# Performance work log

Hardware: AMD Instinct MI355X
Metric: run time of the kernel (lower is better)

Reference implementation:

```python
import jax, jax.numpy as jnp
import numpy as np

B, S, E = 2, 2048, 2048
H = 16
KV_RANK = 512
ROPE = 64
NOPE = 64  # source sets qk_nope_dim = qk_rope_dim
VD = 128   # v_head_dim = head_dim
QD = ROPE + NOPE  # q_head_dim = 128


def setup_inputs() -> dict:
    key = jax.random.key(0)
    ks = jax.random.split(key, 5)
    sd = lambda fan_in: 1.0 / np.sqrt(fan_in)
    return {
        "x": jax.random.normal(ks[0], (B, S, E), jnp.float32),
        "attention_mask": jnp.zeros((1, 1, S, S), jnp.float32),
        "W_kv_down": jax.random.normal(ks[1], (KV_RANK + ROPE, E), jnp.float32) * sd(E),
        "W_kv_up": jax.random.normal(ks[2], (H * (VD + NOPE), KV_RANK), jnp.float32) * sd(KV_RANK),
        "W_q": jax.random.normal(ks[3], (H * QD, E), jnp.float32) * sd(E),
        "W_out": jax.random.normal(ks[4], (E, H * VD), jnp.float32) * sd(H * VD),
    }


def reference(x, attention_mask, W_kv_down, W_kv_up, W_q, W_out):
    scale = QD ** (-0.5)
    # down-project to latent + rope part
    compressed = jnp.einsum('bse,fe->bsf', x, W_kv_down)          # [B,S,KV_RANK+ROPE]
    kv_c, k_rope = compressed[..., :KV_RANK], compressed[..., KV_RANK:]
    # up-project latent to per-head v and k_nope
    kv_exp = jnp.einsum('bsr,fr->bsf', kv_c, W_kv_up)             # [B,S,H*(VD+NOPE)]
    kv_exp = kv_exp.reshape(B, S, H, VD + NOPE).transpose(0, 2, 1, 3)  # [B,H,S,VD+NOPE]
    v, k_nope = kv_exp[..., :VD], kv_exp[..., VD:]
    # shared rope key broadcast over heads, concat [rope, nope]
    k_rope_b = jnp.broadcast_to(k_rope[:, None], (B, H, S, ROPE))
    k = jnp.concatenate([k_rope_b, k_nope], axis=-1)              # [B,H,S,QD]
    # queries
    q = jnp.einsum('bse,fe->bsf', x, W_q).reshape(B, S, H, QD).transpose(0, 2, 1, 3)
    scores = jnp.einsum('bhsd,bhtd->bhst', q, k) * scale + attention_mask
    w = jax.nn.softmax(scores, axis=-1)
    out = jnp.einsum('bhst,bhtv->bhsv', w, v)                     # [B,H,S,VD]
    out = out.transpose(0, 2, 1, 3).reshape(B, S, H * VD)
    return jnp.einsum('bsf,ef->bse', out, W_out)
```

## Files before the change

kernel.cpp:

```cpp
#include <hip/hip_runtime.h>
#include <hip/hip_bf16.h>
#include <stdint.h>

typedef __bf16 bf16x8 __attribute__((ext_vector_type(8)));
typedef float f32x4 __attribute__((ext_vector_type(4)));
typedef unsigned short ushort_t;
typedef unsigned short ushort8v __attribute__((ext_vector_type(8)));

#define MFMA16 __builtin_amdgcn_mfma_f32_16x16x32_bf16

static constexpr int Bc = 2, Sc = 2048, Ec = 2048, Hc = 16;

__device__ __forceinline__ void gload16(const void* g, void* l) {
  __builtin_amdgcn_global_load_lds(
      (const __attribute__((address_space(1))) void*)g,
      (__attribute__((address_space(3))) void*)l, 16, 0, 0);
}

__device__ __forceinline__ ushort_t f2bf(float f) {
  uint32_t u = __float_as_uint(f);
  uint32_t r = (u + 0x7fffu + ((u >> 16) & 1u)) >> 16;
  return (ushort_t)r;
}
__device__ __forceinline__ float bf2f(ushort_t u) {
  return __uint_as_float((uint32_t)u << 16);
}
__device__ __forceinline__ uint32_t cvtpk(float a, float b) {
  uint32_t d;
  asm("v_cvt_pk_bf16_f32 %0, %1, %2" : "=v"(d) : "v"(a), "v"(b));
  return d;
}

__global__ void cast_all(const float* __restrict__ x, const float* __restrict__ Wq,
                         const float* __restrict__ Wkvu, const float* __restrict__ Wout,
                         const float* __restrict__ Wkvd,
                         ushort_t* __restrict__ xb, ushort_t* __restrict__ wq,
                         ushort_t* __restrict__ wkvu, ushort_t* __restrict__ wout,
                         ushort_t* __restrict__ wkvd) {
  int i = blockIdx.x * 256 + threadIdx.x;
  const float* src;
  ushort_t* dst;
  int j;
  if (i < 2097152) { src = x; dst = xb; j = i; }
  else if (i < 3145728) { src = Wq; dst = wq; j = i - 2097152; }
  else if (i < 3538944) { src = Wkvu; dst = wkvu; j = i - 3145728; }
  else if (i < 4587520) { src = Wout; dst = wout; j = i - 3538944; }
  else {
    j = i - 4587520;
    int row = j >> 9, col4 = j & 511;
    ushort4 o;
    if (row < 576) {
      float4 v = ((const float4*)Wkvd)[row * 512 + col4];
      o.x = f2bf(v.x); o.y = f2bf(v.y); o.z = f2bf(v.z); o.w = f2bf(v.w);
    } else { o.x = 0; o.y = 0; o.z = 0; o.w = 0; }
    ((ushort4*)wkvd)[j] = o;
    return;
  }
  float4 v = ((const float4*)src)[j];
  ushort4 o;
  o.x = f2bf(v.x); o.y = f2bf(v.y); o.z = f2bf(v.z); o.w = f2bf(v.w);
  ((ushort4*)dst)[j] = o;
}

__global__ void mask_rearrange(const float* __restrict__ mask, ushort_t* __restrict__ m3) {
  const float INVLN2 = 1.4426950408889634f;
  int i = blockIdx.x * 256 + threadIdx.x;
  if (i >= 524288) return;
  int half = i & 1, g = (i >> 1) & 3, kt = (i >> 3) & 31, q = i >> 8;
  const float* s0 = mask + (size_t)q * 2048 + kt * 64 + half * 32 + g * 4;
  float4 a = *(const float4*)s0;
  float4 c = *(const float4*)(s0 + 16);
  ushort8v o;
  o[0] = f2bf(a.x * INVLN2); o[1] = f2bf(a.y * INVLN2);
  o[2] = f2bf(a.z * INVLN2); o[3] = f2bf(a.w * INVLN2);
  o[4] = f2bf(c.x * INVLN2); o[5] = f2bf(c.y * INVLN2);
  o[6] = f2bf(c.z * INVLN2); o[7] = f2bf(c.w * INVLN2);
  ((ushort8v*)m3)[i] = o;
}

template<int MODE>
__global__ __launch_bounds__(256, 2)
void gemm_bt(const ushort_t* __restrict__ A, int lda,
             const ushort_t* __restrict__ Bm, int ldb,
             void* __restrict__ Cout, int ldc,
             int M, int N, int K,
             char* __restrict__ vtb, char* __restrict__ kbuf)
{
  __shared__ __align__(16) ushort_t sA[128 * 32];
  __shared__ __align__(16) ushort_t sB[128 * 32];
  int tid = threadIdx.x;
  int nTn = N >> 7;
  int bid = blockIdx.x;
  int chunk = gridDim.x >> 3;
  bid = (bid & 7) * chunk + (bid >> 3);
  int tm = bid / nTn, tn = bid - tm * nTn;
  int wave = tid >> 6, lane = tid & 63;
  int wm = (wave >> 1) << 6, wn = (wave & 1) << 6;
  int l16 = lane & 15, g16 = lane >> 4;
  f32x4 acc[4][4] = {};
  int srow = tid >> 2, scol = (tid & 3) << 3;
  const ushort_t* Ag = A + (size_t)(tm * 128 + srow) * lda + scol;
  const ushort_t* Bg = Bm + (size_t)(tn * 128 + srow) * ldb + scol;
  ushort_t* sAp = &sA[srow * 32 + scol];
  ushort_t* sBp = &sB[srow * 32 + scol];
  for (int kt = 0; kt < K; kt += 32) {
    gload16(Ag, sAp);
    gload16(Ag + (size_t)64 * lda, sAp + 64 * 32);
    gload16(Bg, sBp);
    gload16(Bg + (size_t)64 * ldb, sBp + 64 * 32);
    Ag += 32; Bg += 32;
    __syncthreads();
    bf16x8 af[4], bfr[4];
#pragma unroll
    for (int i = 0; i < 4; i++) af[i] = *(const bf16x8*)&sA[(wm + i * 16 + l16) * 32 + g16 * 8];
#pragma unroll
    for (int i = 0; i < 4; i++) bfr[i] = *(const bf16x8*)&sB[(wn + i * 16 + l16) * 32 + g16 * 8];
#pragma unroll
    for (int i = 0; i < 4; i++)
#pragma unroll
      for (int j = 0; j < 4; j++)
        acc[i][j] = MFMA16(af[i], bfr[j], acc[i][j], 0, 0, 0);
    __syncthreads();
  }
#pragma unroll
  for (int i = 0; i < 4; i++) {
#pragma unroll
    for (int j = 0; j < 4; j++) {
#pragma unroll
      for (int r = 0; r < 4; r++) {
        int grow = tm * 128 + wm + i * 16 + g16 * 4 + r;
        int gcol = tn * 128 + wn + j * 16 + l16;
        float v = acc[i][j][r];
        if constexpr (MODE == 0) {
          ((ushort_t*)Cout)[(size_t)grow * ldc + gcol] = f2bf(v);
        } else if constexpr (MODE == 2) {
          ((float*)Cout)[(size_t)grow * ldc + gcol] = v;
        } else {
          int h = gcol / 192, jj = gcol - h * 192;
          int b = grow >> 11, s = grow & 2047;
          size_t bh = (size_t)(b * Hc + h);
          if (jj < 128) {
            *(ushort_t*)(vtb + bh * 524288 + (size_t)jj * 4096 + ((s >> 6) * 128) +
                         ((2 * (s & 63)) ^ ((jj & 7) << 4))) = f2bf(v);
          } else {
            int col = 64 + (jj - 128);
            *(ushort_t*)(kbuf + (bh * Sc + s) * 256 + ((2 * col) ^ ((s & 7) << 4))) = f2bf(v);
          }
        }
      }
    }
  }
}

__global__ void rope_fill(const ushort_t* __restrict__ comp, char* __restrict__ kbuf) {
  int i = blockIdx.x * 256 + threadIdx.x;
  if (i >= Bc * Sc * 8) return;
  int blk = i & 7;
  int m = i >> 3;
  int s = m & 2047, b = m >> 11;
  uint4 v = *(const uint4*)&comp[(size_t)m * 640 + 512 + blk * 8];
  int off = (blk * 16) ^ ((s & 7) << 4);
#pragma unroll
  for (int h = 0; h < Hc; h++) {
    *(uint4*)(kbuf + ((size_t)(b * Hc + h) * Sc + s) * 256 + off) = v;
  }
}

__global__ __launch_bounds__(256, 4)
void attn_kernel(const ushort_t* __restrict__ qb, const char* __restrict__ kbuf,
                 const char* __restrict__ vtb, const ushort_t* __restrict__ m3,
                 ushort_t* __restrict__ attn_o)
{
  __shared__ __align__(16) char smem[40960];
  char* sK = smem;
  char* sV = smem + 16384;
  char* sP = smem + 32768;
  const float scale2 = 0.12752081738040466f;
  int bid = blockIdx.x;
  bid = (bid & 7) * 128 + (bid >> 3);
  int qt = bid & 31, bh = bid >> 5;
  int b = bh >> 4, h = bh & 15;
  int tid = threadIdx.x, wave = tid >> 6, lane = tid & 63;
  int l16 = lane & 15, g16 = lane >> 4;
  int sx = (l16 & 7) << 4;

  bf16x8 qf[4];
  int qrow = qt * 64 + wave * 16 + l16;
  {
    const ushort_t* qp = qb + (size_t)(b * Sc + qrow) * 2048 + h * 128 + g16 * 8;
#pragma unroll
    for (int kf = 0; kf < 4; kf++) qf[kf] = *(const bf16x8*)(qp + kf * 32);
  }

  float mrun = -3.0e38f, lrun = 0.f;
  f32x4 acco[8] = {};

  const char* kg = kbuf + (size_t)bh * Sc * 256;
  const char* vg = vtb + (size_t)bh * 524288;
  char* pB = sP + wave * 2048 + l16 * 128;
  const ushort8v* mq = (const ushort8v*)m3 + (size_t)qrow * 256 + g16 * 2;

  for (int kt = 0; kt < 32; kt++) {
#pragma unroll
    for (int it = 0; it < 4; it++)
      gload16(kg + kt * 16384 + it * 4096 + tid * 16, sK + it * 4096 + tid * 16);
#pragma unroll
    for (int it = 0; it < 4; it++) {
      int l = it * 4096 + tid * 16;
      gload16(vg + (size_t)(l >> 7) * 4096 + kt * 128 + (l & 127), sV + l);
    }
    ushort8v mv0 = mq[kt * 8];
    ushort8v mv1 = mq[kt * 8 + 1];
    __syncthreads();

    f32x4 sc[4] = {};
    __builtin_amdgcn_s_setprio(1);
#pragma unroll
    for (int ni = 0; ni < 4; ni++) {
#pragma unroll
      for (int kf = 0; kf < 4; kf++) {
        bf16x8 kfr = *(const bf16x8*)(sK + (ni * 16 + l16) * 256 +
                                      ((kf * 64 + g16 * 16) ^ sx));
        sc[ni] = MFMA16(kfr, qf[kf], sc[ni], 0, 0, 0);
      }
    }
    __builtin_amdgcn_s_setprio(0);

#pragma unroll
    for (int ni = 0; ni < 4; ni++) {
      const ushort8v& mv = (ni < 2) ? mv0 : mv1;
      int base = (ni & 1) * 4;
#pragma unroll
      for (int r = 0; r < 4; r++)
        sc[ni][r] = sc[ni][r] * scale2 + bf2f(mv[base + r]);
    }
    float mx = fmaxf(fmaxf(fmaxf(sc[0][0], sc[0][1]), fmaxf(sc[0][2], sc[0][3])),
                     fmaxf(fmaxf(sc[1][0], sc[1][1]), fmaxf(sc[1][2], sc[1][3])));
    mx = fmaxf(mx, fmaxf(fmaxf(fmaxf(sc[2][0], sc[2][1]), fmaxf(sc[2][2], sc[2][3])),
                         fmaxf(fmaxf(sc[3][0], sc[3][1]), fmaxf(sc[3][2], sc[3][3]))));
    mx = fmaxf(mx, __shfl_xor(mx, 16));
    mx = fmaxf(mx, __shfl_xor(mx, 32));
    if (!__all(mx <= mrun + 11.0f)) {
      float mnew = fmaxf(mrun, mx);
      float corr = __builtin_amdgcn_exp2f(mrun - mnew);
      lrun *= corr;
      mrun = mnew;
      float cr0 = __shfl(corr, g16 * 4 + 0);
      float cr1 = __shfl(corr, g16 * 4 + 1);
      float cr2 = __shfl(corr, g16 * 4 + 2);
      float cr3 = __shfl(corr, g16 * 4 + 3);
#pragma unroll
      for (int ni = 0; ni < 8; ni++) {
        acco[ni][0] *= cr0; acco[ni][1] *= cr1;
        acco[ni][2] *= cr2; acco[ni][3] *= cr3;
      }
    }
    float rs = 0.f;
#pragma unroll
    for (int ni = 0; ni < 4; ni++) {
      float p0 = __builtin_amdgcn_exp2f(sc[ni][0] - mrun);
      float p1 = __builtin_amdgcn_exp2f(sc[ni][1] - mrun);
      float p2 = __builtin_amdgcn_exp2f(sc[ni][2] - mrun);
      float p3 = __builtin_amdgcn_exp2f(sc[ni][3] - mrun);
      rs += (p0 + p1) + (p2 + p3);
      uint2 w;
      w.x = cvtpk(p0, p1);
      w.y = cvtpk(p2, p3);
      *(uint2*)(pB + ((ni * 32 + g16 * 8) ^ sx)) = w;
    }
    lrun += rs;

    __builtin_amdgcn_s_setprio(1);
#pragma unroll
    for (int kf = 0; kf < 2; kf++) {
      bf16x8 pa = *(const bf16x8*)(pB + ((kf * 64 + g16 * 16) ^ sx));
#pragma unroll
      for (int ni = 0; ni < 8; ni++) {
        bf16x8 vf = *(const bf16x8*)(sV + (ni * 16 + l16) * 128 +
                                     ((kf * 64 + g16 * 16) ^ sx));
        acco[ni] = MFMA16(pa, vf, acco[ni], 0, 0, 0);
      }
    }
    __builtin_amdgcn_s_setprio(0);

    __syncthreads();
  }

  lrun += __shfl_xor(lrun, 16);
  lrun += __shfl_xor(lrun, 32);
  float lr[4];
#pragma unroll
  for (int r = 0; r < 4; r++) lr[r] = __shfl(lrun, g16 * 4 + r);
#pragma unroll
  for (int ni = 0; ni < 8; ni++) {
#pragma unroll
    for (int r = 0; r < 4; r++) {
      int qr = qt * 64 + wave * 16 + g16 * 4 + r;
      int col = ni * 16 + l16;
      float o = acco[ni][r] / lr[r];
      attn_o[(size_t)(b * Sc + qr) * 2048 + h * 128 + col] = f2bf(o);
    }
  }
}

extern "C" void kernel_launch(void* const* d_in, const int* in_sizes, int n_in,
                              void* d_out, int out_size, void* d_ws, size_t ws_size,
                              hipStream_t stream) {
  const float* x    = (const float*)d_in[0];
  const float* mask = (const float*)d_in[1];
  const float* Wkvd = (const float*)d_in[2];
  const float* Wkvu = (const float*)d_in[3];
  const float* Wq   = (const float*)d_in[4];
  const float* Wout = (const float*)d_in[5];

  char* ws = (char*)d_ws;
  size_t off = 0;
  auto alloc = [&](size_t bytes) { char* p = ws + off; off += (bytes + 255) & ~(size_t)255; return p; };
  ushort_t* xb   = (ushort_t*)alloc((size_t)4096 * 2048 * 2);
  ushort_t* wkvd = (ushort_t*)alloc((size_t)640 * 2048 * 2);
  ushort_t* wq   = (ushort_t*)alloc((size_t)2048 * 2048 * 2);
  ushort_t* wkvu = (ushort_t*)alloc((size_t)3072 * 512 * 2);
  ushort_t* wout = (ushort_t*)alloc((size_t)2048 * 2048 * 2);
  ushort_t* comp = (ushort_t*)alloc((size_t)4096 * 640 * 2);
  ushort_t* qbuf = (ushort_t*)alloc((size_t)4096 * 2048 * 2);
  char*     kbuf = alloc((size_t)Bc * Hc * Sc * 256);
  char*     vtb  = alloc((size_t)Bc * Hc * 524288);
  ushort_t* attn_o = xb;
  ushort_t* m3 = wq;

  cast_all<<<19200, 256, 0, stream>>>(x, Wq, Wkvu, Wout, Wkvd, xb, wq, wkvu, wout, wkvd);

  gemm_bt<0><<<32 * 5, 256, 0, stream>>>(xb, 2048, wkvd, 2048, comp, 640, 4096, 640, 2048, nullptr, nullptr);
  gemm_bt<0><<<32 * 16, 256, 0, stream>>>(xb, 2048, wq, 2048, qbuf, 2048, 4096, 2048, 2048, nullptr, nullptr);
  mask_rearrange<<<2048, 256, 0, stream>>>(mask, m3);
  gemm_bt<1><<<32 * 24, 256, 0, stream>>>(comp, 640, wkvu, 512, nullptr, 0, 4096, 3072, 512, vtb, kbuf);
  rope_fill<<<32768 / 256, 256, 0, stream>>>(comp, kbuf);
  attn_kernel<<<1024, 256, 0, stream>>>(qbuf, kbuf, vtb, m3, attn_o);
  gemm_bt<2><<<32 * 16, 256, 0, stream>>>(attn_o, 2048, wout, 2048, d_out, 2048, 4096, 2048, 2048, nullptr, nullptr);
}
```

Baseline: 294.2 us.

## Rework attention kernel to 32x32 MFMA with register-resident P via permlane swap

The attention kernel moves from 16x16x32 to 32x32x16 bf16 MFMA tiles. Each wave now owns 32 query rows, and the block shrinks to 2 waves (128 threads). The softmax probabilities stay in registers and are rearranged with v_permlane32_swap instead of a round trip through shared memory, which removes the P LDS buffer and its writes and reads. The mask rearrangement is changed to match the new accumulator layout. The trade-off is fewer waves per block, larger accumulators with more register pressure, and a launch bound of 2 that may lower occupancy.

```diff
diff --git a/kernel.cpp b/kernel.cpp
--- a/kernel.cpp
+++ b/kernel.cpp
@@ -4,10 +4,13 @@
 
 typedef __bf16 bf16x8 __attribute__((ext_vector_type(8)));
 typedef float f32x4 __attribute__((ext_vector_type(4)));
+typedef float f32x16 __attribute__((ext_vector_type(16)));
+typedef uint32_t u32x4 __attribute__((ext_vector_type(4)));
 typedef unsigned short ushort_t;
 typedef unsigned short ushort8v __attribute__((ext_vector_type(8)));
 
 #define MFMA16 __builtin_amdgcn_mfma_f32_16x16x32_bf16
+#define MFMA32 __builtin_amdgcn_mfma_f32_32x32x16_bf16
 
 static constexpr int Bc = 2, Sc = 2048, Ec = 2048, Hc = 16;
 
@@ -29,6 +32,9 @@
   uint32_t d;
   asm("v_cvt_pk_bf16_f32 %0, %1, %2" : "=v"(d) : "v"(a), "v"(b));
   return d;
+}
+__device__ __forceinline__ void plswap(uint32_t& a, uint32_t& b) {
+  asm("v_permlane32_swap_b32 %0, %1" : "+v"(a), "+v"(b));
 }
 
 __global__ void cast_all(const float* __restrict__ x, const float* __restrict__ Wq,
@@ -62,20 +68,20 @@
   ((ushort4*)dst)[j] = o;
 }
 
-__global__ void mask_rearrange(const float* __restrict__ mask, ushort_t* __restrict__ m3) {
+__global__ void mask_rearrange(const float* __restrict__ mask, ushort_t* __restrict__ m4) {
   const float INVLN2 = 1.4426950408889634f;
   int i = blockIdx.x * 256 + threadIdx.x;
   if (i >= 524288) return;
-  int half = i & 1, g = (i >> 1) & 3, kt = (i >> 3) & 31, q = i >> 8;
-  const float* s0 = mask + (size_t)q * 2048 + kt * 64 + half * 32 + g * 4;
-  float4 a = *(const float4*)s0;
-  float4 c = *(const float4*)(s0 + 16);
+  int rr = i & 1, half = (i >> 1) & 1, kblk = (i >> 2) & 1, kt = (i >> 3) & 31, q = i >> 8;
+  const float* src = mask + (size_t)q * 2048 + kt * 64 + kblk * 32 + half * 4 + rr * 16;
+  float4 a = *(const float4*)src;
+  float4 c = *(const float4*)(src + 8);
   ushort8v o;
   o[0] = f2bf(a.x * INVLN2); o[1] = f2bf(a.y * INVLN2);
   o[2] = f2bf(a.z * INVLN2); o[3] = f2bf(a.w * INVLN2);
   o[4] = f2bf(c.x * INVLN2); o[5] = f2bf(c.y * INVLN2);
   o[6] = f2bf(c.z * INVLN2); o[7] = f2bf(c.w * INVLN2);
-  ((ushort8v*)m3)[i] = o;
+  ((ushort8v*)m4)[i] = o;
 }
 
 template<int MODE>
@@ -166,140 +172,136 @@
   }
 }
 
-__global__ __launch_bounds__(256, 4)
+__global__ __launch_bounds__(128, 2)
 void attn_kernel(const ushort_t* __restrict__ qb, const char* __restrict__ kbuf,
-                 const char* __restrict__ vtb, const ushort_t* __restrict__ m3,
+                 const char* __restrict__ vtb, const ushort_t* __restrict__ m4,
                  ushort_t* __restrict__ attn_o)
 {
-  __shared__ __align__(16) char smem[40960];
+  __shared__ __align__(16) char smem[32768];
   char* sK = smem;
   char* sV = smem + 16384;
-  char* sP = smem + 32768;
   const float scale2 = 0.12752081738040466f;
   int bid = blockIdx.x;
   bid = (bid & 7) * 128 + (bid >> 3);
   int qt = bid & 31, bh = bid >> 5;
   int b = bh >> 4, h = bh & 15;
   int tid = threadIdx.x, wave = tid >> 6, lane = tid & 63;
-  int l16 = lane & 15, g16 = lane >> 4;
-  int sx = (l16 & 7) << 4;
-
-  bf16x8 qf[4];
-  int qrow = qt * 64 + wave * 16 + l16;
+  int l32 = lane & 31, half = lane >> 5;
+  int sx = (l32 & 7) << 4;
+  int qbase = qt * 64 + wave * 32;
+
+  bf16x8 qf[8];
   {
-    const ushort_t* qp = qb + (size_t)(b * Sc + qrow) * 2048 + h * 128 + g16 * 8;
-#pragma unroll
-    for (int kf = 0; kf < 4; kf++) qf[kf] = *(const bf16x8*)(qp + kf * 32);
+    const ushort_t* qp = qb + (size_t)(b * Sc + qbase + l32) * 2048 + h * 128 + half * 8;
+#pragma unroll
+    for (int ks = 0; ks < 8; ks++) qf[ks] = *(const bf16x8*)(qp + ks * 16);
   }
 
   float mrun = -3.0e38f, lrun = 0.f;
-  f32x4 acco[8] = {};
-
-  const char* kg = kbuf + (size_t)bh * Sc * 256;
+  f32x16 acco[4] = {};
+
+  const char* kg = kbuf + (size_t)bh * 524288;
   const char* vg = vtb + (size_t)bh * 524288;
-  char* pB = sP + wave * 2048 + l16 * 128;
-  const ushort8v* mq = (const ushort8v*)m3 + (size_t)qrow * 256 + g16 * 2;
+  const ushort8v* mq = (const ushort8v*)m4 + (size_t)(qbase + l32) * 256 + half * 2;
 
   for (int kt = 0; kt < 32; kt++) {
 #pragma unroll
-    for (int it = 0; it < 4; it++)
-      gload16(kg + kt * 16384 + it * 4096 + tid * 16, sK + it * 4096 + tid * 16);
-#pragma unroll
-    for (int it = 0; it < 4; it++) {
-      int l = it * 4096 + tid * 16;
+    for (int it = 0; it < 8; it++)
+      gload16(kg + kt * 16384 + it * 2048 + tid * 16, sK + it * 2048 + tid * 16);
+#pragma unroll
+    for (int it = 0; it < 8; it++) {
+      int l = it * 2048 + tid * 16;
       gload16(vg + (size_t)(l >> 7) * 4096 + kt * 128 + (l & 127), sV + l);
     }
-    ushort8v mv0 = mq[kt * 8];
-    ushort8v mv1 = mq[kt * 8 + 1];
+    ushort8v mvv[4];
+#pragma unroll
+    for (int kb = 0; kb < 2; kb++)
+#pragma unroll
+      for (int rr = 0; rr < 2; rr++)
+        mvv[kb * 2 + rr] = mq[kt * 8 + kb * 4 + rr];
     __syncthreads();
 
-    f32x4 sc[4] = {};
-    __builtin_amdgcn_s_setprio(1);
-#pragma unroll
-    for (int ni = 0; ni < 4; ni++) {
-#pragma unroll
-      for (int kf = 0; kf < 4; kf++) {
-        bf16x8 kfr = *(const bf16x8*)(sK + (ni * 16 + l16) * 256 +
-                                      ((kf * 64 + g16 * 16) ^ sx));
-        sc[ni] = MFMA16(kfr, qf[kf], sc[ni], 0, 0, 0);
-      }
+#pragma unroll
+    for (int kblk = 0; kblk < 2; kblk++) {
+      f32x16 sc = {};
+      __builtin_amdgcn_s_setprio(1);
+#pragma unroll
+      for (int ks = 0; ks < 8; ks++) {
+        bf16x8 kfr = *(const bf16x8*)(sK + (kblk * 32 + l32) * 256 +
+                                      ((ks * 32 + half * 16) ^ sx));
+        sc = MFMA32(kfr, qf[ks], sc, 0, 0, 0);
+      }
+      __builtin_amdgcn_s_setprio(0);
+
+#pragma unroll
+      for (int r = 0; r < 16; r++)
+        sc[r] = sc[r] * scale2 + bf2f(mvv[kblk * 2 + (r >> 3)][r & 7]);
+      float mx = sc[0];
+#pragma unroll
+      for (int r = 1; r < 16; r++) mx = fmaxf(mx, sc[r]);
+      mx = fmaxf(mx, __shfl_xor(mx, 32));
+      if (!__all(mx <= mrun + 11.0f)) {
+        float mnew = fmaxf(mrun, mx);
+        float corr = __builtin_amdgcn_exp2f(mrun - mnew);
+        lrun *= corr; mrun = mnew;
+#pragma unroll
+        for (int r = 0; r < 16; r++) {
+          float cr = __shfl(corr, (r & 3) + 8 * (r >> 2) + 4 * half);
+#pragma unroll
+          for (int vb = 0; vb < 4; vb++) acco[vb][r] *= cr;
+        }
+      }
+      float rs = 0.f;
+      uint32_t W[8];
+#pragma unroll
+      for (int m = 0; m < 4; m++) {
+        float p0 = __builtin_amdgcn_exp2f(sc[4 * m + 0] - mrun);
+        float p1 = __builtin_amdgcn_exp2f(sc[4 * m + 1] - mrun);
+        float p2 = __builtin_amdgcn_exp2f(sc[4 * m + 2] - mrun);
+        float p3 = __builtin_amdgcn_exp2f(sc[4 * m + 3] - mrun);
+        rs += (p0 + p1) + (p2 + p3);
+        W[2 * m] = cvtpk(p0, p1);
+        W[2 * m + 1] = cvtpk(p2, p3);
+      }
+      lrun += rs;
+
+      bf16x8 pf[2];
+#pragma unroll
+      for (int k2 = 0; k2 < 2; k2++) {
+        uint32_t a0 = W[4 * k2 + 0], a1 = W[4 * k2 + 1];
+        uint32_t b0 = W[4 * k2 + 2], b1 = W[4 * k2 + 3];
+        plswap(a0, b0);
+        plswap(a1, b1);
+        u32x4 t; t[0] = a0; t[1] = a1; t[2] = b0; t[3] = b1;
+        pf[k2] = __builtin_bit_cast(bf16x8, t);
+      }
+
+      __builtin_amdgcn_s_setprio(1);
+#pragma unroll
+      for (int k2 = 0; k2 < 2; k2++)
+#pragma unroll
+        for (int vb = 0; vb < 4; vb++) {
+          bf16x8 vf = *(const bf16x8*)(sV + (vb * 32 + l32) * 128 +
+                                       ((kblk * 64 + k2 * 32 + half * 16) ^ sx));
+          acco[vb] = MFMA32(pf[k2], vf, acco[vb], 0, 0, 0);
+        }
+      __builtin_amdgcn_s_setprio(0);
     }
-    __builtin_amdgcn_s_setprio(0);
-
-#pragma unroll
-    for (int ni = 0; ni < 4; ni++) {
-      const ushort8v& mv = (ni < 2) ? mv0 : mv1;
-      int base = (ni & 1) * 4;
-#pragma unroll
-      for (int r = 0; r < 4; r++)
-        sc[ni][r] = sc[ni][r] * scale2 + bf2f(mv[base + r]);
-    }
-    float mx = fmaxf(fmaxf(fmaxf(sc[0][0], sc[0][1]), fmaxf(sc[0][2], sc[0][3])),
-                     fmaxf(fmaxf(sc[1][0], sc[1][1]), fmaxf(sc[1][2], sc[1][3])));
-    mx = fmaxf(mx, fmaxf(fmaxf(fmaxf(sc[2][0], sc[2][1]), fmaxf(sc[2][2], sc[2][3])),
-                         fmaxf(fmaxf(sc[3][0], sc[3][1]), fmaxf(sc[3][2], sc[3][3]))));
-    mx = fmaxf(mx, __shfl_xor(mx, 16));
-    mx = fmaxf(mx, __shfl_xor(mx, 32));
-    if (!__all(mx <= mrun + 11.0f)) {
-      float mnew = fmaxf(mrun, mx);
-      float corr = __builtin_amdgcn_exp2f(mrun - mnew);
-      lrun *= corr;
-      mrun = mnew;
-      float cr0 = __shfl(corr, g16 * 4 + 0);
-      float cr1 = __shfl(corr, g16 * 4 + 1);
-      float cr2 = __shfl(corr, g16 * 4 + 2);
-      float cr3 = __shfl(corr, g16 * 4 + 3);
-#pragma unroll
-      for (int ni = 0; ni < 8; ni++) {
-        acco[ni][0] *= cr0; acco[ni][1] *= cr1;
-        acco[ni][2] *= cr2; acco[ni][3] *= cr3;
-      }
-    }
-    float rs = 0.f;
-#pragma unroll
-    for (int ni = 0; ni < 4; ni++) {
-      float p0 = __builtin_amdgcn_exp2f(sc[ni][0] - mrun);
-      float p1 = __builtin_amdgcn_exp2f(sc[ni][1] - mrun);
-      float p2 = __builtin_amdgcn_exp2f(sc[ni][2] - mrun);
-      float p3 = __builtin_amdgcn_exp2f(sc[ni][3] - mrun);
-      rs += (p0 + p1) + (p2 + p3);
-      uint2 w;
-      w.x = cvtpk(p0, p1);
-      w.y = cvtpk(p2, p3);
-      *(uint2*)(pB + ((ni * 32 + g16 * 8) ^ sx)) = w;
-    }
-    lrun += rs;
-
-    __builtin_amdgcn_s_setprio(1);
-#pragma unroll
-    for (int kf = 0; kf < 2; kf++) {
-      bf16x8 pa = *(const bf16x8*)(pB + ((kf * 64 + g16 * 16) ^ sx));
-#pragma unroll
-      for (int ni = 0; ni < 8; ni++) {
-        bf16x8 vf = *(const bf16x8*)(sV + (ni * 16 + l16) * 128 +
-                                     ((kf * 64 + g16 * 16) ^ sx));
-        acco[ni] = MFMA16(pa, vf, acco[ni], 0, 0, 0);
-      }
-    }
-    __builtin_amdgcn_s_setprio(0);
 
     __syncthreads();
   }
 
-  lrun += __shfl_xor(lrun, 16);
   lrun += __shfl_xor(lrun, 32);
-  float lr[4];
-#pragma unroll
-  for (int r = 0; r < 4; r++) lr[r] = __shfl(lrun, g16 * 4 + r);
-#pragma unroll
-  for (int ni = 0; ni < 8; ni++) {
-#pragma unroll
-    for (int r = 0; r < 4; r++) {
-      int qr = qt * 64 + wave * 16 + g16 * 4 + r;
-      int col = ni * 16 + l16;
-      float o = acco[ni][r] / lr[r];
-      attn_o[(size_t)(b * Sc + qr) * 2048 + h * 128 + col] = f2bf(o);
-    }
+#pragma unroll
+  for (int r = 0; r < 16; r++) {
+    int rowq = (r & 3) + 8 * (r >> 2) + 4 * half;
+    float lr = __shfl(lrun, rowq);
+    float inv = 1.0f / lr;
+    int qrow = qbase + rowq;
+    ushort_t* op = attn_o + (size_t)(b * Sc + qrow) * 2048 + h * 128 + l32;
+#pragma unroll
+    for (int vb = 0; vb < 4; vb++)
+      op[vb * 32] = f2bf(acco[vb][r] * inv);
   }
 }
 
@@ -326,15 +328,15 @@
   char*     kbuf = alloc((size_t)Bc * Hc * Sc * 256);
   char*     vtb  = alloc((size_t)Bc * Hc * 524288);
   ushort_t* attn_o = xb;
-  ushort_t* m3 = wq;
+  ushort_t* m4 = wq;
 
   cast_all<<<19200, 256, 0, stream>>>(x, Wq, Wkvu, Wout, Wkvd, xb, wq, wkvu, wout, wkvd);
 
   gemm_bt<0><<<32 * 5, 256, 0, stream>>>(xb, 2048, wkvd, 2048, comp, 640, 4096, 640, 2048, nullptr, nullptr);
   gemm_bt<0><<<32 * 16, 256, 0, stream>>>(xb, 2048, wq, 2048, qbuf, 2048, 4096, 2048, 2048, nullptr, nullptr);
-  mask_rearrange<<<2048, 256, 0, stream>>>(mask, m3);
+  mask_rearrange<<<2048, 256, 0, stream>>>(mask, m4);
   gemm_bt<1><<<32 * 24, 256, 0, stream>>>(comp, 640, wkvu, 512, nullptr, 0, 4096, 3072, 512, vtb, kbuf);
   rope_fill<<<32768 / 256, 256, 0, stream>>>(comp, kbuf);
-  attn_kernel<<<1024, 256, 0, stream>>>(qbuf, kbuf, vtb, m3, attn_o);
+  attn_kernel<<<1024, 128, 0, stream>>>(qbuf, kbuf, vtb, m4, attn_o);
   gemm_bt<2><<<32 * 16, 256, 0, stream>>>(attn_o, 2048, wout, 2048, d_out, 2048, 4096, 2048, 2048, nullptr, nullptr);
 }
```

Measured after the change: 288.9 us. About the same (-1.8%).
